# Performance work log

Hardware: AMD Instinct MI355X
Metric: run time of the kernel (lower is better)

The kernel has to match this reference:

```python
import jax, jax.numpy as jnp
import numpy as np

C = 2048
N = 8
K = C // N  # 256
B = 4096


def setup_inputs() -> dict:
    key = jax.random.key(0)
    ks = jax.random.split(key, 9)
    s_in = 1.0 / np.sqrt(C)
    s_k = 1.0 / np.sqrt(K)
    return {
        "x": jax.random.normal(ks[0], (B, C), dtype=jnp.float32),
        # weights stored [in, out] (y = x @ W + b), equivalent to torch Linear
        "W_theta": jax.random.uniform(ks[1], (C, K), jnp.float32, -s_in, s_in),
        "b_theta": jax.random.uniform(ks[2], (K,), jnp.float32, -s_in, s_in),
        "W_phi": jax.random.uniform(ks[3], (C, K), jnp.float32, -s_in, s_in),
        "b_phi": jax.random.uniform(ks[4], (K,), jnp.float32, -s_in, s_in),
        "W_f": jax.random.uniform(ks[5], (C, K), jnp.float32, -s_in, s_in),
        "b_f": jax.random.uniform(ks[6], (K,), jnp.float32, -s_in, s_in),
        "W_g": jax.random.uniform(ks[7], (K, C), jnp.float32, -s_k, s_k),
        "b_g": jax.random.uniform(ks[8], (C,), jnp.float32, -s_k, s_k),
    }


def reference(x, W_theta, b_theta, W_phi, b_phi, W_f, b_f, W_g, b_g):
    theta = x @ W_theta + b_theta          # [B, K]
    phi = x @ W_phi + b_phi                # [B, K]
    f = x @ W_f + b_f                      # [B, K]
    # outer product per sample -> [B, K, K], softmax over last dim
    scores = jax.nn.softmax(theta[:, :, None] * phi[:, None, :], axis=-1)
    t = jnp.einsum('bij,bj->bi', scores, f)  # [B, K]
    return x + t @ W_g + b_g               # residual, [B, C]
```

## Files before the change

### kernel.cpp

```cpp
#include <hip/hip_runtime.h>

constexpr int Bsz   = 4096;
constexpr int Cdim  = 2048;
constexpr int Kdim  = 256;
constexpr int PROJW = 3 * Kdim;
constexpr int KSPLIT = 4;

typedef __attribute__((ext_vector_type(8))) short short8;
typedef __attribute__((ext_vector_type(4))) float floatx4;
typedef __attribute__((ext_vector_type(2))) float float2v;
typedef __attribute__((ext_vector_type(4))) _Float16 half4v;

__device__ __forceinline__ unsigned short f2bf(float f) {
    unsigned int u = __float_as_uint(f);
    u += 0x7FFFu + ((u >> 16) & 1u);
    return (unsigned short)(u >> 16);
}

__device__ __forceinline__ void load16(const void* g, void* lds) {
    __builtin_amdgcn_global_load_lds(
        (const __attribute__((address_space(1))) unsigned int*)g,
        (__attribute__((address_space(3))) unsigned int*)lds, 16, 0, 0);
}


__global__ __launch_bounds__(256) void prep_kernel(
    const float* __restrict__ x, unsigned short* __restrict__ xb2,
    const float* __restrict__ Wt, const float* __restrict__ Wp,
    const float* __restrict__ Wf, const float* __restrict__ Wg,
    unsigned short* __restrict__ Wcat2, unsigned short* __restrict__ WgT)
{
    __shared__ float tile[32][33];
    const int bid = blockIdx.x;
    if (bid < 8192) {
        const int i   = bid * 256 + threadIdx.x;
        const int row = i >> 9;
        const int kq  = i & 511;
        float4 v = reinterpret_cast<const float4*>(x)[i];
        ushort4 o;
        o.x = f2bf(v.x); o.y = f2bf(v.y); o.z = f2bf(v.z); o.w = f2bf(v.w);
        const size_t dst = ((size_t)(row >> 7) * 64 + (kq >> 3)) * 4096 +
                           (row & 127) * 32 + (kq & 7) * 4;
        *reinterpret_cast<ushort4*>(xb2 + dst) = o;
        return;
    }
    const int q = bid - 8192;
    const int z = q >> 9;
    const int tileId = q & 511;
    const float* __restrict__ in;
    int R, C;
    if (z < 3) {
        in = (z == 0) ? Wt : (z == 1) ? Wp : Wf;
        R = Cdim; C = Kdim;
    } else {
        in = Wg; R = Kdim; C = Cdim;
    }
    const int ctiles = C / 32;
    const int c0 = (tileId % ctiles) * 32;
    const int r0 = (tileId / ctiles) * 32;
    const int tx = threadIdx.x & 31, ty = threadIdx.x >> 5;
#pragma unroll
    for (int i = ty; i < 32; i += 8)
        tile[i][tx] = in[(size_t)(r0 + i) * C + c0 + tx];
    __syncthreads();
    if (z < 3) {
#pragma unroll
        for (int i = ty; i < 32; i += 8) {
            const int cg = z * 256 + c0 + i;
            Wcat2[((size_t)(cg >> 7) * 64 + (r0 >> 5)) * 4096 +
                  (cg & 127) * 32 + tx] = f2bf(tile[tx][i]);
        }
    } else {
#pragma unroll
        for (int i = ty; i < 32; i += 8)
            WgT[(size_t)(c0 + i) * R + r0 + tx] = f2bf(tile[tx][i]);
    }
}

constexpr int RPS = 152;

__global__ __launch_bounds__(256) void proj_mfma(
    const unsigned short* __restrict__ xb2,
    const unsigned short* __restrict__ Wcat2,
    _Float16* __restrict__ pp)
{
    __shared__ __align__(16) char pool[128 * RPS * 2];
    short* As = (short*)pool;
    short* Bs = As + 128 * 32;

    const int tid  = threadIdx.x;
    const int lane = tid & 63;
    const int wid  = tid >> 6;
    const int wr   = wid >> 1, wc = wid & 1;
    const int rowBase = blockIdx.x * 128;
    const int colBase = blockIdx.y * 128;

    floatx4 acc[4][4] = {};

    const unsigned short* gA =
        xb2 + ((size_t)blockIdx.x * 64 + blockIdx.z * 16) * 4096 + tid * 8;
    const unsigned short* gB =
        Wcat2 + ((size_t)blockIdx.y * 64 + blockIdx.z * 16) * 4096 + tid * 8;

    short* ldsA0 = As + ((tid & ~63)) * 8;
    short* ldsA1 = As + (256 + (tid & ~63)) * 8;
    short* ldsB0 = Bs + ((tid & ~63)) * 8;
    short* ldsB1 = Bs + (256 + (tid & ~63)) * 8;

    const int mrow = lane & 15;
    const int kgrp = lane >> 4;

    for (int kt = 0; kt < 16; ++kt) {
        load16(gA, ldsA0); load16(gA + 2048, ldsA1);
        load16(gB, ldsB0); load16(gB + 2048, ldsB1);
        gA += 4096; gB += 4096;
        __syncthreads();

        short8 af[4], bfr[4];
#pragma unroll
        for (int i = 0; i < 4; ++i)
            af[i]  = *(const short8*)&As[(wr * 64 + i * 16 + mrow) * 32 + kgrp * 8];
#pragma unroll
        for (int j = 0; j < 4; ++j)
            bfr[j] = *(const short8*)&Bs[(wc * 64 + j * 16 + mrow) * 32 + kgrp * 8];
#pragma unroll
        for (int i = 0; i < 4; ++i)
#pragma unroll
            for (int j = 0; j < 4; ++j)
                acc[i][j] = __builtin_amdgcn_mfma_f32_16x16x32_bf16(
                    af[i], bfr[j], acc[i][j], 0, 0, 0);
        __syncthreads();
    }

    _Float16* rp = (_Float16*)pool;
#pragma unroll
    for (int j = 0; j < 4; ++j) {
        const int cL = wc * 64 + j * 16 + mrow;
#pragma unroll
        for (int i = 0; i < 4; ++i)
#pragma unroll
            for (int r = 0; r < 4; ++r)
                rp[(wr * 64 + i * 16 + kgrp * 4 + r) * RPS + cL] =
                    (_Float16)acc[i][j][r];
    }
    __syncthreads();

    _Float16* __restrict__ dst = pp + (size_t)blockIdx.z * Bsz * PROJW;
#pragma unroll
    for (int it = 0; it < 8; ++it) {
        const int c    = it * 256 + tid;
        const int rowL = c >> 4;
        const int ch   = c & 15;
        const float4 v = *reinterpret_cast<const float4*>(&rp[rowL * RPS + ch * 8]);
        *reinterpret_cast<float4*>(
            &dst[(size_t)(rowBase + rowL) * PROJW + colBase + ch * 8]) = v;
    }
}

__global__ __launch_bounds__(256) void attn_kernel(
    const _Float16* __restrict__ pp,
    const float* __restrict__ bt, const float* __restrict__ bp,
    const float* __restrict__ bff,
    unsigned short* __restrict__ t)
{
    __shared__ float sphi[4][Kdim];
    __shared__ float sff[4][Kdim];

    const int tid = threadIdx.x;
    const int s   = tid >> 6;
    const int l   = tid & 63;
    const int b   = blockIdx.x * 4 + s;
    const int j0  = l * 4;
    const size_t rowOff = (size_t)b * PROJW;

    float4 th = *reinterpret_cast<const float4*>(bt + j0);
    float4 ph = *reinterpret_cast<const float4*>(bp + j0);
    float4 fv = *reinterpret_cast<const float4*>(bff + j0);
#pragma unroll
    for (int z = 0; z < KSPLIT; ++z) {
        const _Float16* __restrict__ r = pp + (size_t)z * Bsz * PROJW + rowOff;
        half4v a = *reinterpret_cast<const half4v*>(r + j0);
        half4v c = *reinterpret_cast<const half4v*>(r + Kdim + j0);
        half4v d = *reinterpret_cast<const half4v*>(r + 2 * Kdim + j0);
        th.x += (float)a.x; th.y += (float)a.y; th.z += (float)a.z; th.w += (float)a.w;
        ph.x += (float)c.x; ph.y += (float)c.y; ph.z += (float)c.z; ph.w += (float)c.w;
        fv.x += (float)d.x; fv.y += (float)d.y; fv.z += (float)d.z; fv.w += (float)d.w;
    }
    const float tl[4] = {th.x * 1.44269504f, th.y * 1.44269504f,
                         th.z * 1.44269504f, th.w * 1.44269504f};
    *reinterpret_cast<float4*>(&sphi[s][j0]) = ph;
    *reinterpret_cast<float4*>(&sff[s][j0])  = fv;
    __syncthreads();

    float2v sa[4][2] = {}, na[4][2] = {};
    const float4* __restrict__ sp  = reinterpret_cast<const float4*>(sphi[s]);
    const float4* __restrict__ sfp = reinterpret_cast<const float4*>(sff[s]);
#pragma unroll 4
    for (int p = 0; p < Kdim / 4; ++p) {
        const float4 ph4 = sp[p];
        const float4 ff4 = sfp[p];
        const float2v p01 = {ph4.x, ph4.y};
        const float2v p23 = {ph4.z, ph4.w};
        const float2v f01 = {ff4.x, ff4.y};
        const float2v f23 = {ff4.z, ff4.w};
#pragma unroll
        for (int i = 0; i < 4; ++i) {
            const float2v a01 = tl[i] * p01;
            const float2v a23 = tl[i] * p23;
            float2v e01, e23;
            e01.x = __builtin_amdgcn_exp2f(a01.x);
            e01.y = __builtin_amdgcn_exp2f(a01.y);
            e23.x = __builtin_amdgcn_exp2f(a23.x);
            e23.y = __builtin_amdgcn_exp2f(a23.y);
            sa[i][0] += e01;
            sa[i][1] += e23;
            na[i][0] += e01 * f01;
            na[i][1] += e23 * f23;
        }
    }
    ushort4 o;
    unsigned short* op = &o.x;
#pragma unroll
    for (int i = 0; i < 4; ++i) {
        const float den = sa[i][0].x + sa[i][0].y + sa[i][1].x + sa[i][1].y;
        const float num = na[i][0].x + na[i][0].y + na[i][1].x + na[i][1].y;
        op[i] = f2bf(num * __builtin_amdgcn_rcpf(den));
    }
    *reinterpret_cast<ushort4*>(t + (size_t)b * Kdim + j0) = o;
}

constexpr int OPS = 68;

__global__ __launch_bounds__(256) void out_mfma(
    const unsigned short* __restrict__ tb,
    const unsigned short* __restrict__ WgT,
    const float* __restrict__ bg,
    const float* __restrict__ x,
    float* __restrict__ out)
{
    __shared__ __align__(16) char pool[128 * OPS * 4];
    short* As = (short*)pool;
    short* Bs = As + 128 * 32;

    const int tid  = threadIdx.x;
    const int lane = tid & 63;
    const int wid  = tid >> 6;
    const int wr   = wid >> 1, wc = wid & 1;
    const int rowBase = blockIdx.x * 128;
    const int colBase = blockIdx.y * 128;

    floatx4 acc[4][4] = {};

    const unsigned short* gA0 = tb  + (size_t)(rowBase + (tid >> 2)) * Kdim + (tid & 3) * 8;
    const unsigned short* gA1 = tb  + (size_t)(rowBase + 64 + (tid >> 2)) * Kdim + (tid & 3) * 8;
    const unsigned short* gB0 = WgT + (size_t)(colBase + (tid >> 2)) * Kdim + (tid & 3) * 8;
    const unsigned short* gB1 = WgT + (size_t)(colBase + 64 + (tid >> 2)) * Kdim + (tid & 3) * 8;

    short* ldsA0 = As + ((tid & ~63)) * 8;
    short* ldsA1 = As + (256 + (tid & ~63)) * 8;
    short* ldsB0 = Bs + ((tid & ~63)) * 8;
    short* ldsB1 = Bs + (256 + (tid & ~63)) * 8;

    const int mrow = lane & 15;
    const int kgrp = lane >> 4;

    for (int kt = 0; kt < Kdim; kt += 32) {
        load16(gA0, ldsA0); load16(gA1, ldsA1);
        load16(gB0, ldsB0); load16(gB1, ldsB1);
        gA0 += 32; gA1 += 32; gB0 += 32; gB1 += 32;
        __syncthreads();

        short8 af[4], bfr[4];
#pragma unroll
        for (int i = 0; i < 4; ++i)
            af[i]  = *(const short8*)&As[(wr * 64 + i * 16 + mrow) * 32 + kgrp * 8];
#pragma unroll
        for (int j = 0; j < 4; ++j)
            bfr[j] = *(const short8*)&Bs[(wc * 64 + j * 16 + mrow) * 32 + kgrp * 8];
#pragma unroll
        for (int i = 0; i < 4; ++i)
#pragma unroll
            for (int j = 0; j < 4; ++j)
                acc[i][j] = __builtin_amdgcn_mfma_f32_16x16x32_bf16(
                    af[i], bfr[j], acc[i][j], 0, 0, 0);
        __syncthreads();
    }

    float* rp = (float*)pool;
#pragma unroll
    for (int h = 0; h < 2; ++h) {
        if (wc == h) {
#pragma unroll
            for (int j = 0; j < 4; ++j) {
                const int cL = j * 16 + mrow;
#pragma unroll
                for (int i = 0; i < 4; ++i)
#pragma unroll
                    for (int r = 0; r < 4; ++r)
                        rp[(wr * 64 + i * 16 + kgrp * 4 + r) * OPS + cL] =
                            acc[i][j][r];
            }
        }
        __syncthreads();
#pragma unroll
        for (int it = 0; it < 8; ++it) {
            const int c    = it * 256 + tid;
            const int rowL = c >> 4;
            const int ch   = c & 15;
            const float4 v = *reinterpret_cast<const float4*>(&rp[rowL * OPS + ch * 4]);
            const int colG = colBase + h * 64 + ch * 4;
            const size_t g = (size_t)(rowBase + rowL) * Cdim + colG;
            const float4 bgv = *reinterpret_cast<const float4*>(bg + colG);
            const float4 xv  = *reinterpret_cast<const float4*>(x + g);
            float4 o;
            o.x = v.x + bgv.x + xv.x;
            o.y = v.y + bgv.y + xv.y;
            o.z = v.z + bgv.z + xv.z;
            o.w = v.w + bgv.w + xv.w;
            *reinterpret_cast<float4*>(out + g) = o;
        }
        __syncthreads();
    }
}

extern "C" void kernel_launch(void* const* d_in, const int* in_sizes, int n_in,
                              void* d_out, int out_size, void* d_ws, size_t ws_size,
                              hipStream_t stream) {
    const float* x  = (const float*)d_in[0];
    const float* Wt = (const float*)d_in[1];
    const float* bt = (const float*)d_in[2];
    const float* Wp = (const float*)d_in[3];
    const float* bp = (const float*)d_in[4];
    const float* Wf = (const float*)d_in[5];
    const float* bf = (const float*)d_in[6];
    const float* Wg = (const float*)d_in[7];
    const float* bg = (const float*)d_in[8];
    float* out = (float*)d_out;

    char* w = (char*)d_ws;
    _Float16*       pp    = (_Float16*)w;
    unsigned short* xb2   = (unsigned short*)(w + 25165824);
    unsigned short* Wcat2 = (unsigned short*)(w + 41943040);
    unsigned short* WgT   = (unsigned short*)(w + 45088768);
    unsigned short* tb    = (unsigned short*)(w + 46137344);

    prep_kernel<<<10240, 256, 0, stream>>>(x, xb2, Wt, Wp, Wf, Wg, Wcat2, WgT);
    proj_mfma<<<dim3(Bsz / 128, PROJW / 128, KSPLIT), 256, 0, stream>>>(xb2, Wcat2, pp);
    attn_kernel<<<Bsz / 4, 256, 0, stream>>>(pp, bt, bp, bf, tb);
    out_mfma<<<dim3(Bsz / 128, Cdim / 128), 256, 0, stream>>>(tb, WgT, bg, x, out);
}
```

Baseline: 163.5 us.

## Halve GEMM barriers with 64-wide K chunks and read residual from bf16 copy

Both MFMA GEMMs now stage two 32-wide K slices per barrier pair, halving synchronisation count. The output epilogue reads the residual from the bf16 tiled copy of x instead of fp32 x, halving that read traffic. The prep kernel converts x in larger per-block tiles with fewer blocks. The residual now carries bf16 rounding error, which may affect accuracy tolerance.

```diff
diff --git a/kernel.cpp b/kernel.cpp
--- a/kernel.cpp
+++ b/kernel.cpp
@@ -15,6 +15,9 @@
     unsigned int u = __float_as_uint(f);
     u += 0x7FFFu + ((u >> 16) & 1u);
     return (unsigned short)(u >> 16);
+}
+__device__ __forceinline__ float bf2f(unsigned short b) {
+    return __uint_as_float((unsigned int)b << 16);
 }
 
 __device__ __forceinline__ void load16(const void* g, void* lds) {
@@ -32,19 +35,23 @@
 {
     __shared__ float tile[32][33];
     const int bid = blockIdx.x;
-    if (bid < 8192) {
-        const int i   = bid * 256 + threadIdx.x;
-        const int row = i >> 9;
-        const int kq  = i & 511;
-        float4 v = reinterpret_cast<const float4*>(x)[i];
-        ushort4 o;
-        o.x = f2bf(v.x); o.y = f2bf(v.y); o.z = f2bf(v.z); o.w = f2bf(v.w);
-        const size_t dst = ((size_t)(row >> 7) * 64 + (kq >> 3)) * 4096 +
-                           (row & 127) * 32 + (kq & 7) * 4;
-        *reinterpret_cast<ushort4*>(xb2 + dst) = o;
+    if (bid < 2048) {
+        const int rt = bid >> 6, kt = bid & 63;
+        const int r  = threadIdx.x >> 1, h = threadIdx.x & 1;
+        const float* __restrict__ src =
+            x + (size_t)(rt * 128 + r) * Cdim + kt * 32 + h * 16;
+        unsigned short* __restrict__ dst =
+            xb2 + ((size_t)rt * 64 + kt) * 4096 + r * 32 + h * 16;
+#pragma unroll
+        for (int q = 0; q < 4; ++q) {
+            const float4 v = reinterpret_cast<const float4*>(src)[q];
+            ushort4 o;
+            o.x = f2bf(v.x); o.y = f2bf(v.y); o.z = f2bf(v.z); o.w = f2bf(v.w);
+            reinterpret_cast<ushort4*>(dst)[q] = o;
+        }
         return;
     }
-    const int q = bid - 8192;
+    const int q = bid - 2048;
     const int z = q >> 9;
     const int tileId = q & 511;
     const float* __restrict__ in;
@@ -86,7 +93,7 @@
 {
     __shared__ __align__(16) char pool[128 * RPS * 2];
     short* As = (short*)pool;
-    short* Bs = As + 128 * 32;
+    short* Bs = As + 2 * 4096;
 
     const int tid  = threadIdx.x;
     const int lane = tid & 63;
@@ -102,33 +109,35 @@
     const unsigned short* gB =
         Wcat2 + ((size_t)blockIdx.y * 64 + blockIdx.z * 16) * 4096 + tid * 8;
 
-    short* ldsA0 = As + ((tid & ~63)) * 8;
-    short* ldsA1 = As + (256 + (tid & ~63)) * 8;
-    short* ldsB0 = Bs + ((tid & ~63)) * 8;
-    short* ldsB1 = Bs + (256 + (tid & ~63)) * 8;
-
+    const int wbase = (tid & ~63) * 8;
     const int mrow = lane & 15;
     const int kgrp = lane >> 4;
 
-    for (int kt = 0; kt < 16; ++kt) {
-        load16(gA, ldsA0); load16(gA + 2048, ldsA1);
-        load16(gB, ldsB0); load16(gB + 2048, ldsB1);
-        gA += 4096; gB += 4096;
-        __syncthreads();
-
-        short8 af[4], bfr[4];
-#pragma unroll
-        for (int i = 0; i < 4; ++i)
-            af[i]  = *(const short8*)&As[(wr * 64 + i * 16 + mrow) * 32 + kgrp * 8];
-#pragma unroll
-        for (int j = 0; j < 4; ++j)
-            bfr[j] = *(const short8*)&Bs[(wc * 64 + j * 16 + mrow) * 32 + kgrp * 8];
-#pragma unroll
-        for (int i = 0; i < 4; ++i)
+    for (int kt = 0; kt < 8; ++kt) {
+#pragma unroll
+        for (int c = 0; c < 4; ++c) {
+            load16(gA + c * 2048, As + c * 2048 + wbase);
+            load16(gB + c * 2048, Bs + c * 2048 + wbase);
+        }
+        gA += 8192; gB += 8192;
+        __syncthreads();
+
+#pragma unroll
+        for (int s = 0; s < 2; ++s) {
+            short8 af[4], bfr[4];
+#pragma unroll
+            for (int i = 0; i < 4; ++i)
+                af[i]  = *(const short8*)&As[s * 4096 + (wr * 64 + i * 16 + mrow) * 32 + kgrp * 8];
 #pragma unroll
             for (int j = 0; j < 4; ++j)
-                acc[i][j] = __builtin_amdgcn_mfma_f32_16x16x32_bf16(
-                    af[i], bfr[j], acc[i][j], 0, 0, 0);
+                bfr[j] = *(const short8*)&Bs[s * 4096 + (wc * 64 + j * 16 + mrow) * 32 + kgrp * 8];
+#pragma unroll
+            for (int i = 0; i < 4; ++i)
+#pragma unroll
+                for (int j = 0; j < 4; ++j)
+                    acc[i][j] = __builtin_amdgcn_mfma_f32_16x16x32_bf16(
+                        af[i], bfr[j], acc[i][j], 0, 0, 0);
+        }
         __syncthreads();
     }
 
@@ -235,12 +244,12 @@
     const unsigned short* __restrict__ tb,
     const unsigned short* __restrict__ WgT,
     const float* __restrict__ bg,
-    const float* __restrict__ x,
+    const unsigned short* __restrict__ xb2,
     float* __restrict__ out)
 {
     __shared__ __align__(16) char pool[128 * OPS * 4];
     short* As = (short*)pool;
-    short* Bs = As + 128 * 32;
+    short* Bs = As + 2 * 4096;
 
     const int tid  = threadIdx.x;
     const int lane = tid & 63;
@@ -251,38 +260,45 @@
 
     floatx4 acc[4][4] = {};
 
-    const unsigned short* gA0 = tb  + (size_t)(rowBase + (tid >> 2)) * Kdim + (tid & 3) * 8;
-    const unsigned short* gA1 = tb  + (size_t)(rowBase + 64 + (tid >> 2)) * Kdim + (tid & 3) * 8;
-    const unsigned short* gB0 = WgT + (size_t)(colBase + (tid >> 2)) * Kdim + (tid & 3) * 8;
-    const unsigned short* gB1 = WgT + (size_t)(colBase + 64 + (tid >> 2)) * Kdim + (tid & 3) * 8;
-
-    short* ldsA0 = As + ((tid & ~63)) * 8;
-    short* ldsA1 = As + (256 + (tid & ~63)) * 8;
-    short* ldsB0 = Bs + ((tid & ~63)) * 8;
-    short* ldsB1 = Bs + (256 + (tid & ~63)) * 8;
-
+    const int srow = tid >> 2;
+    const int skq  = (tid & 3) * 8;
+    const unsigned short* gA0 = tb  + (size_t)(rowBase + srow) * Kdim + skq;
+    const unsigned short* gA1 = tb  + (size_t)(rowBase + 64 + srow) * Kdim + skq;
+    const unsigned short* gB0 = WgT + (size_t)(colBase + srow) * Kdim + skq;
+    const unsigned short* gB1 = WgT + (size_t)(colBase + 64 + srow) * Kdim + skq;
+
+    const int wbase = (tid & ~63) * 8;
     const int mrow = lane & 15;
     const int kgrp = lane >> 4;
 
-    for (int kt = 0; kt < Kdim; kt += 32) {
-        load16(gA0, ldsA0); load16(gA1, ldsA1);
-        load16(gB0, ldsB0); load16(gB1, ldsB1);
-        gA0 += 32; gA1 += 32; gB0 += 32; gB1 += 32;
-        __syncthreads();
-
-        short8 af[4], bfr[4];
-#pragma unroll
-        for (int i = 0; i < 4; ++i)
-            af[i]  = *(const short8*)&As[(wr * 64 + i * 16 + mrow) * 32 + kgrp * 8];
-#pragma unroll
-        for (int j = 0; j < 4; ++j)
-            bfr[j] = *(const short8*)&Bs[(wc * 64 + j * 16 + mrow) * 32 + kgrp * 8];
-#pragma unroll
-        for (int i = 0; i < 4; ++i)
+    for (int kt = 0; kt < Kdim; kt += 64) {
+        load16(gA0, As + wbase);
+        load16(gA1, As + 2048 + wbase);
+        load16(gB0, Bs + wbase);
+        load16(gB1, Bs + 2048 + wbase);
+        load16(gA0 + 32, As + 4096 + wbase);
+        load16(gA1 + 32, As + 4096 + 2048 + wbase);
+        load16(gB0 + 32, Bs + 4096 + wbase);
+        load16(gB1 + 32, Bs + 4096 + 2048 + wbase);
+        gA0 += 64; gA1 += 64; gB0 += 64; gB1 += 64;
+        __syncthreads();
+
+#pragma unroll
+        for (int s = 0; s < 2; ++s) {
+            short8 af[4], bfr[4];
+#pragma unroll
+            for (int i = 0; i < 4; ++i)
+                af[i]  = *(const short8*)&As[s * 4096 + (wr * 64 + i * 16 + mrow) * 32 + kgrp * 8];
 #pragma unroll
             for (int j = 0; j < 4; ++j)
-                acc[i][j] = __builtin_amdgcn_mfma_f32_16x16x32_bf16(
-                    af[i], bfr[j], acc[i][j], 0, 0, 0);
+                bfr[j] = *(const short8*)&Bs[s * 4096 + (wc * 64 + j * 16 + mrow) * 32 + kgrp * 8];
+#pragma unroll
+            for (int i = 0; i < 4; ++i)
+#pragma unroll
+                for (int j = 0; j < 4; ++j)
+                    acc[i][j] = __builtin_amdgcn_mfma_f32_16x16x32_bf16(
+                        af[i], bfr[j], acc[i][j], 0, 0, 0);
+        }
         __syncthreads();
     }
 
@@ -310,13 +326,15 @@
             const float4 v = *reinterpret_cast<const float4*>(&rp[rowL * OPS + ch * 4]);
             const int colG = colBase + h * 64 + ch * 4;
             const size_t g = (size_t)(rowBase + rowL) * Cdim + colG;
+            const size_t xoff = ((size_t)blockIdx.x * 64 + (colG >> 5)) * 4096 +
+                                rowL * 32 + (colG & 31);
+            const ushort4 xv4 = *reinterpret_cast<const ushort4*>(xb2 + xoff);
             const float4 bgv = *reinterpret_cast<const float4*>(bg + colG);
-            const float4 xv  = *reinterpret_cast<const float4*>(x + g);
             float4 o;
-            o.x = v.x + bgv.x + xv.x;
-            o.y = v.y + bgv.y + xv.y;
-            o.z = v.z + bgv.z + xv.z;
-            o.w = v.w + bgv.w + xv.w;
+            o.x = v.x + bgv.x + bf2f(xv4.x);
+            o.y = v.y + bgv.y + bf2f(xv4.y);
+            o.z = v.z + bgv.z + bf2f(xv4.z);
+            o.w = v.w + bgv.w + bf2f(xv4.w);
             *reinterpret_cast<float4*>(out + g) = o;
         }
         __syncthreads();
@@ -344,8 +362,8 @@
     unsigned short* WgT   = (unsigned short*)(w + 45088768);
     unsigned short* tb    = (unsigned short*)(w + 46137344);
 
-    prep_kernel<<<10240, 256, 0, stream>>>(x, xb2, Wt, Wp, Wf, Wg, Wcat2, WgT);
+    prep_kernel<<<4096, 256, 0, stream>>>(x, xb2, Wt, Wp, Wf, Wg, Wcat2, WgT);
     proj_mfma<<<dim3(Bsz / 128, PROJW / 128, KSPLIT), 256, 0, stream>>>(xb2, Wcat2, pp);
     attn_kernel<<<Bsz / 4, 256, 0, stream>>>(pp, bt, bp, bf, tb);
-    out_mfma<<<dim3(Bsz / 128, Cdim / 128), 256, 0, stream>>>(tb, WgT, bg, x, out);
-}
+    out_mfma<<<dim3(Bsz / 128, Cdim / 128), 256, 0, stream>>>(tb, WgT, bg, xb2, out);
+}
```

Measured after the change: 168.9 us. +3.3%, slower.
